# Optimization experiments

Hardware: AMD Instinct MI355X
Metric: run time of the kernel (lower is better)

Reference implementation:

```python
import jax, jax.numpy as jnp
import numpy as np

H = 4  # num_heads (hard-coded in module)
RATION = 5


def setup_inputs() -> dict:
    key = jax.random.key(0)
    ks = jax.random.split(key, 14)
    B, T, S, F = 256, 5, 64, 256
    u = 0.05  # keras 'uniform' initializer scale
    d = {}
    d["x"] = jax.random.normal(ks[0], (B, T, S, F), jnp.float32)
    d["atten_bias"] = jax.random.uniform(ks[1], (B, T, S, S), jnp.float32) * 0.1
    d["W_q"] = jax.random.uniform(ks[2], (F, F), jnp.float32, -u, u)
    d["W_v"] = jax.random.uniform(ks[3], (F, F), jnp.float32, -u, u)
    d["W_o"] = jax.random.uniform(ks[4], (F, F), jnp.float32, -u, u)
    d["u_t"] = jax.random.uniform(ks[5], (T,), jnp.float32, -u, u)
    d["dis"] = jax.random.uniform(ks[6], (T, S, S), jnp.float32, -u, u)
    # keep sigma away from 0 to avoid blowing up the Gaussian prior
    d["sigma"] = jax.random.uniform(ks[7], (T, S, 1), jnp.float32, 0.5, 1.0)
    # SE block: fc1 Dense(T*RATION, relu, he_normal), fc2 Dense(T, sigmoid)
    d["fc1_w"] = jax.random.normal(ks[8], (T, T * RATION), jnp.float32) * np.sqrt(2.0 / T).astype(np.float32)
    d["fc1_b"] = jnp.zeros((T * RATION,), jnp.float32)
    d["fc2_w"] = jax.random.normal(ks[9], (T * RATION, T), jnp.float32) * np.sqrt(2.0 / (T * RATION)).astype(np.float32)
    d["fc2_b"] = jnp.zeros((T,), jnp.float32)
    d["bili_w"] = jax.random.uniform(ks[10], (1,), jnp.float32, -u, u)
    return d


def _se_block(o, fc1_w, fc1_b, fc2_w, fc2_b, bili_w):
    # o: [B,T,S,F] -> transpose to [B,S,F,T]; "channel" axis is T
    xt = jnp.transpose(o, (0, 2, 3, 1))
    avg = jnp.mean(xt, axis=(1, 2))  # [B,T]
    mx = jnp.max(xt, axis=(1, 2))    # [B,T]
    se1 = jax.nn.sigmoid(jax.nn.relu(avg @ fc1_w + fc1_b) @ fc2_w + fc2_b)
    se2 = jax.nn.sigmoid(jax.nn.relu(mx @ fc1_w + fc1_b) @ fc2_w + fc2_b)
    w = bili_w  # shape (1,)
    se = (1.0 - w) * se1 + w * se2   # [B,T]
    out = xt * se[:, None, None, :]
    return jnp.transpose(out, (0, 3, 1, 2))  # back to [B,T,S,F]


def reference(x, atten_bias, W_q, W_v, W_o, u_t, dis, sigma, fc1_w, fc1_b, fc2_w, fc2_b, bili_w):
    B, T, S, F = x.shape
    Fh = F // H
    # q, v: project then reshape (row-major split, exactly as TF reshape)
    q = (x @ W_q).reshape(-1, T, S, Fh)          # [H*B, T, S, Fh]
    v = (x @ W_v).reshape(-1, T, S, Fh)          # [H*B, T, S, Fh]
    # k: contract time with u_t, then [B,F,S] -> [H*B, Fh, S]
    k = jnp.einsum('t,btsf->bsf', u_t, x)        # [B, S, F]
    k = jnp.transpose(k, (0, 2, 1)).reshape(-1, Fh, S)  # [H*B, Fh, S]
    score = jnp.einsum('btsf,bfc->btsc', q, k) / jnp.sqrt(jnp.asarray(Fh, x.dtype))
    score = jax.nn.sigmoid(score)                # [H*B, T, S, S]
    score = score - jnp.tile(atten_bias, (H, 1, 1, 1))
    # learned spatial Gaussian prior, broadcast over batch
    prior = (1.0 / (jnp.sqrt(2.0 * jnp.pi) * sigma)) * jnp.exp(-dis ** 2 / (2.0 * sigma ** 2))
    score = score * prior
    # Dropout(0.3) is identity at inference
    score = jnp.sum(score, axis=-2)              # [H*B, T, S]
    atten = v * score[..., None]                 # [H*B, T, S, Fh]
    o = atten.reshape(-1, T, S, F) @ W_o         # [B, T, S, F]
    o = _se_block(o, fc1_w, fc1_b, fc2_w, fc2_b, bili_w)
    return o + x
```

## Files before the change

kernel.cpp:

```cpp
#include <hip/hip_runtime.h>


typedef unsigned short ushort_t;
typedef __attribute__((ext_vector_type(8))) short bf16x8;
typedef __attribute__((ext_vector_type(4))) float f32x4;

__device__ inline ushort_t f2bf(float f) {
  unsigned u = __float_as_uint(f);
  return (ushort_t)((u + 0x7FFFu + ((u >> 16) & 1u)) >> 16);
}
__device__ inline float bflo(unsigned u) { return __uint_as_float(u << 16); }
__device__ inline float bfhi(unsigned u) { return __uint_as_float(u & 0xFFFF0000u); }

__global__ __launch_bounds__(256) void prior_kernel(const float* __restrict__ dis,
                                                    const float* __restrict__ sigma,
                                                    float* __restrict__ prior) {
  int i = blockIdx.x * 256 + threadIdx.x;
  if (i >= 5 * 64 * 64) return;
  int ts = i >> 6;
  float sg = sigma[ts];
  float d = dis[i];
  prior[i] = 0.3989422804014327f / sg * __expf(-d * d / (2.f * sg * sg));
}

__global__ __launch_bounds__(256) void bias_prior_sum(const float* __restrict__ bias,
                                                      const float* __restrict__ prior,
                                                      float* __restrict__ bps) {
  int blk = blockIdx.x;
  int t = blk % 5, tid = threadIdx.x;
  const float* bp = bias + (size_t)blk * 4096;
  const float* pp = prior + t * 4096;
  int c = tid & 63, sg = tid >> 6;
  float sum = 0.f;
  for (int s = sg * 16; s < sg * 16 + 16; ++s)
    sum += bp[s * 64 + c] * pp[s * 64 + c];
  __shared__ float red[4][64];
  red[sg][c] = sum;
  __syncthreads();
  if (tid < 64)
    bps[(size_t)blk * 64 + tid] = red[0][tid] + red[1][tid] + red[2][tid] + red[3][tid];
}

__global__ __launch_bounds__(256) void k_kernel(const float* __restrict__ x,
                                                const float* __restrict__ u,
                                                ushort_t* __restrict__ kout,
                                                ushort_t* __restrict__ xb) {
  int i = blockIdx.x * 256 + threadIdx.x;
  size_t j = (size_t)i * 4;
  int b = (int)(j >> 14);
  int off = (int)(j & 16383);
  const float* xp = x + (size_t)b * 81920 + off;
  ushort_t* xq = xb + (size_t)b * 81920 + off;
  float u0 = u[0], u1 = u[1], u2 = u[2], u3 = u[3], u4 = u[4];
  float4 a0 = *(const float4*)(xp);
  float4 a1 = *(const float4*)(xp + 16384);
  float4 a2 = *(const float4*)(xp + 32768);
  float4 a3 = *(const float4*)(xp + 49152);
  float4 a4 = *(const float4*)(xp + 65536);
  ushort4 h0 = {f2bf(a0.x), f2bf(a0.y), f2bf(a0.z), f2bf(a0.w)};
  ushort4 h1 = {f2bf(a1.x), f2bf(a1.y), f2bf(a1.z), f2bf(a1.w)};
  ushort4 h2 = {f2bf(a2.x), f2bf(a2.y), f2bf(a2.z), f2bf(a2.w)};
  ushort4 h3 = {f2bf(a3.x), f2bf(a3.y), f2bf(a3.z), f2bf(a3.w)};
  ushort4 h4 = {f2bf(a4.x), f2bf(a4.y), f2bf(a4.z), f2bf(a4.w)};
  *(ushort4*)(xq) = h0;
  *(ushort4*)(xq + 16384) = h1;
  *(ushort4*)(xq + 32768) = h2;
  *(ushort4*)(xq + 49152) = h3;
  *(ushort4*)(xq + 65536) = h4;
  float4 r;
  r.x = u0 * a0.x + u1 * a1.x + u2 * a2.x + u3 * a3.x + u4 * a4.x;
  r.y = u0 * a0.y + u1 * a1.y + u2 * a2.y + u3 * a3.y + u4 * a4.y;
  r.z = u0 * a0.z + u1 * a1.z + u2 * a2.z + u3 * a3.z + u4 * a4.z;
  r.w = u0 * a0.w + u1 * a1.w + u2 * a2.w + u3 * a3.w + u4 * a4.w;
  ushort4 h = {f2bf(r.x), f2bf(r.y), f2bf(r.z), f2bf(r.w)};
  *(ushort4*)(kout + j) = h;
}

__global__ __launch_bounds__(256) void convert_w(const float* __restrict__ Wq,
                                                 const float* __restrict__ Wv,
                                                 const float* __restrict__ Wo,
                                                 ushort_t* __restrict__ Wt) {
  int id = blockIdx.x * 256 + threadIdx.x;
  if (id >= 196608) return;
  int mat = id >> 16, rem = id & 65535;
  int n = rem >> 8, k = rem & 255;
  const float* W = mat == 0 ? Wq : (mat == 1 ? Wv : Wo);
  Wt[id] = f2bf(W[k * 256 + n]);
}

template<int SCALE, int SEEPI>
__global__ __launch_bounds__(512, 4) void gemm_mfma(
    const ushort_t* __restrict__ A, const ushort_t* __restrict__ Wt,
    ushort_t* __restrict__ C, const float* __restrict__ ssum,
    float* __restrict__ ravg, float* __restrict__ rmax) {
  __shared__ __align__(16) ushort_t As_[128 * 64];
  __shared__ __align__(16) ushort_t Bs_[256 * 64];
  __shared__ float redS[8], redM[8];
  const int tid = threadIdx.x;
  const int lane = tid & 63;
  const int w = tid >> 6, wr = w >> 2, wc = w & 3;
  const int row0 = blockIdx.x * 128;
  const int cl = lane & 15, ql = lane >> 4, l7 = lane & 7;

  f32x4 acc[4][4];
#pragma unroll
  for (int i = 0; i < 4; ++i)
#pragma unroll
    for (int j = 0; j < 4; ++j) acc[i][j] = (f32x4){0.f, 0.f, 0.f, 0.f};

  for (int t = 0; t < 4; ++t) {
    const int k0 = t * 64;
    if (t) __syncthreads();
#pragma unroll
    for (int l = 0; l < 2; ++l) {
      int i = l * 512 + tid;
      int r = i >> 3, c = i & 7;
      uint4 v = *(const uint4*)(A + (size_t)(row0 + r) * 256 + k0 + c * 8);
      *(uint4*)&As_[r * 64 + ((c ^ (r & 7)) * 8)] = v;
    }
#pragma unroll
    for (int l = 0; l < 4; ++l) {
      int i = l * 512 + tid;
      int n = i >> 3, c = i & 7;
      uint4 v = *(const uint4*)(Wt + (size_t)n * 256 + k0 + c * 8);
      *(uint4*)&Bs_[n * 64 + ((c ^ (n & 7)) * 8)] = v;
    }
    __syncthreads();
#pragma unroll
    for (int kk = 0; kk < 2; ++kk) {
      const int offk = (((kk << 2) | ql) ^ l7) * 8;
      bf16x8 bfr[4], afr[4];
#pragma unroll
      for (int ni = 0; ni < 4; ++ni)
        bfr[ni] = *(const bf16x8*)&Bs_[(wc * 64 + ni * 16 + cl) * 64 + offk];
#pragma unroll
      for (int mi = 0; mi < 4; ++mi)
        afr[mi] = *(const bf16x8*)&As_[(wr * 64 + mi * 16 + cl) * 64 + offk];
#pragma unroll
      for (int mi = 0; mi < 4; ++mi)
#pragma unroll
        for (int ni = 0; ni < 4; ++ni)
          acc[mi][ni] = __builtin_amdgcn_mfma_f32_16x16x32_bf16(afr[mi], bfr[ni], acc[mi][ni], 0, 0, 0);
    }
  }
  float lsum = 0.f, lmax = -3.4e38f;
#pragma unroll
  for (int mi = 0; mi < 4; ++mi) {
    float sc[4];
    if (SCALE) {
#pragma unroll
      for (int r = 0; r < 4; ++r)
        sc[r] = ssum[(size_t)(row0 + wr * 64 + mi * 16 + ql * 4 + r) * 4 + wc];
    }
#pragma unroll
    for (int ni = 0; ni < 4; ++ni) {
      int col = wc * 64 + ni * 16 + cl;
      f32x4 v = acc[mi][ni];
#pragma unroll
      for (int r = 0; r < 4; ++r) {
        int row = row0 + wr * 64 + mi * 16 + ql * 4 + r;
        float f = v[r];
        if (SCALE) f *= sc[r];
        C[(size_t)row * 256 + col] = f2bf(f);
        if (SEEPI) { lsum += f; lmax = fmaxf(lmax, f); }
      }
    }
  }
  if (SEEPI) {
#pragma unroll
    for (int off = 32; off; off >>= 1) {
      lsum += __shfl_xor(lsum, off);
      lmax = fmaxf(lmax, __shfl_xor(lmax, off));
    }
    if (lane == 0) { redS[w] = lsum; redM[w] = lmax; }
    __syncthreads();
    if (tid < 2) {
      float s = redS[tid * 4] + redS[tid * 4 + 1] + redS[tid * 4 + 2] + redS[tid * 4 + 3];
      float m = fmaxf(fmaxf(redM[tid * 4], redM[tid * 4 + 1]),
                      fmaxf(redM[tid * 4 + 2], redM[tid * 4 + 3]));
      ravg[blockIdx.x * 2 + tid] = s * (1.f / 16384.f);
      rmax[blockIdx.x * 2 + tid] = m;
    }
  }
}

__global__ __launch_bounds__(256) void score_mfma(const ushort_t* __restrict__ q,
                                                  const ushort_t* __restrict__ kbuf,
                                                  const float* __restrict__ prior,
                                                  const float* __restrict__ bps,
                                                  float* __restrict__ ssum) {
  const int n = blockIdx.x;
  const int tid = threadIdx.x;
  const int lane = tid & 63;
  const int w = tid >> 6;
  const int cl = lane & 15, ql = lane >> 4;
  const int nb = n & 255;
  const int c = w * 16 + cl;
  const ushort_t* kb = kbuf + (size_t)(n >> 2) * 16384 + (n & 3) * 64;
  bf16x8 kfr0 = *(const bf16x8*)(kb + c * 256 + ql * 8);
  bf16x8 kfr1 = *(const bf16x8*)(kb + c * 256 + ql * 8 + 32);
  for (int t = 0; t < 5; ++t) {
    const ushort_t* qt = q + (size_t)n * 20480 + t * 4096;
    f32x4 acc[4];
#pragma unroll
    for (int si = 0; si < 4; ++si) {
      bf16x8 a0 = *(const bf16x8*)(qt + (si * 16 + cl) * 64 + ql * 8);
      bf16x8 a1 = *(const bf16x8*)(qt + (si * 16 + cl) * 64 + ql * 8 + 32);
      f32x4 z = (f32x4){0.f, 0.f, 0.f, 0.f};
      z = __builtin_amdgcn_mfma_f32_16x16x32_bf16(a0, kfr0, z, 0, 0, 0);
      z = __builtin_amdgcn_mfma_f32_16x16x32_bf16(a1, kfr1, z, 0, 0, 0);
      acc[si] = z;
    }
    const float* pp = prior + t * 4096;
    float colsum = 0.f;
#pragma unroll
    for (int si = 0; si < 4; ++si) {
#pragma unroll
      for (int r = 0; r < 4; ++r) {
        int s = si * 16 + ql * 4 + r;
        float sg = 1.f / (1.f + __expf(-acc[si][r] * 0.125f));
        colsum += sg * pp[s * 64 + c];
      }
    }
    colsum += __shfl_xor(colsum, 16);
    colsum += __shfl_xor(colsum, 32);
    if (ql == 0)
      ssum[(size_t)n * 320 + t * 64 + c] = colsum - bps[((size_t)nb * 5 + t) * 64 + c];
  }
}

__global__ __launch_bounds__(256) void se_mlp(const float* __restrict__ ravg,
                                              const float* __restrict__ rmax,
                                              const float* __restrict__ fc1w,
                                              const float* __restrict__ fc1b,
                                              const float* __restrict__ fc2w,
                                              const float* __restrict__ fc2b,
                                              const float* __restrict__ bili,
                                              float* __restrict__ se) {
  int b = threadIdx.x;
  float avg[5], mx[5];
  for (int t = 0; t < 5; ++t) { avg[t] = ravg[b * 5 + t]; mx[t] = rmax[b * 5 + t]; }
  float w = bili[0];
  float h[25], s1[5], s2[5];
  for (int j = 0; j < 25; ++j) {
    float a = fc1b[j];
    for (int t = 0; t < 5; ++t) a += avg[t] * fc1w[t * 25 + j];
    h[j] = fmaxf(a, 0.f);
  }
  for (int t = 0; t < 5; ++t) {
    float a = fc2b[t];
    for (int j = 0; j < 25; ++j) a += h[j] * fc2w[j * 5 + t];
    s1[t] = 1.f / (1.f + __expf(-a));
  }
  for (int j = 0; j < 25; ++j) {
    float a = fc1b[j];
    for (int t = 0; t < 5; ++t) a += mx[t] * fc1w[t * 25 + j];
    h[j] = fmaxf(a, 0.f);
  }
  for (int t = 0; t < 5; ++t) {
    float a = fc2b[t];
    for (int j = 0; j < 25; ++j) a += h[j] * fc2w[j * 5 + t];
    s2[t] = 1.f / (1.f + __expf(-a));
  }
  for (int t = 0; t < 5; ++t) se[b * 5 + t] = (1.f - w) * s1[t] + w * s2[t];
}

__global__ __launch_bounds__(256) void final_kernel(const float* __restrict__ x,
                                                    const float* __restrict__ se,
                                                    const ushort_t* __restrict__ ob,
                                                    float* __restrict__ out) {
  int i = blockIdx.x * 256 + threadIdx.x;
  size_t j = (size_t)i * 4;
  int bt = (int)(j >> 14);
  float s = se[bt];
  uint2 u = *(const uint2*)(ob + j);
  float4 xv = *(const float4*)(x + j);
  float4 r = {bflo(u.x) * s + xv.x, bfhi(u.x) * s + xv.y,
              bflo(u.y) * s + xv.z, bfhi(u.y) * s + xv.w};
  *(float4*)(out + j) = r;
}

extern "C" void kernel_launch(void* const* d_in, const int* in_sizes, int n_in,
                              void* d_out, int out_size, void* d_ws, size_t ws_size,
                              hipStream_t stream) {
  const float* x     = (const float*)d_in[0];
  const float* bias  = (const float*)d_in[1];
  const float* Wq    = (const float*)d_in[2];
  const float* Wv    = (const float*)d_in[3];
  const float* Wo    = (const float*)d_in[4];
  const float* u_t   = (const float*)d_in[5];
  const float* dis   = (const float*)d_in[6];
  const float* sigma = (const float*)d_in[7];
  const float* fc1w  = (const float*)d_in[8];
  const float* fc1b  = (const float*)d_in[9];
  const float* fc2w  = (const float*)d_in[10];
  const float* fc2b  = (const float*)d_in[11];
  const float* bili  = (const float*)d_in[12];
  float* out = (float*)d_out;

  char* wsb = (char*)d_ws;
  ushort_t* qvb  = (ushort_t*)wsb;             wsb += 41943040;
  ushort_t* xob  = (ushort_t*)wsb;             wsb += 41943040;
  ushort_t* kb   = (ushort_t*)wsb;             wsb += 8388608;
  ushort_t* Wt   = (ushort_t*)wsb;             wsb += 393216;
  float*    ssum = (float*)wsb;                wsb += 1310720;
  float*    prior= (float*)wsb;                wsb += 81920;
  float*    bps  = (float*)wsb;                wsb += 327680;
  float*    ravg = (float*)wsb;                wsb += 5120;
  float*    rmax = (float*)wsb;                wsb += 5120;
  float*    se   = (float*)wsb;                wsb += 5120;

  convert_w<<<768, 256, 0, stream>>>(Wq, Wv, Wo, Wt);
  prior_kernel<<<80, 256, 0, stream>>>(dis, sigma, prior);
  bias_prior_sum<<<1280, 256, 0, stream>>>(bias, prior, bps);
  k_kernel<<<4096, 256, 0, stream>>>(x, u_t, kb, xob);
  gemm_mfma<0, 0><<<640, 512, 0, stream>>>(xob, Wt, qvb, nullptr, nullptr, nullptr);
  score_mfma<<<1024, 256, 0, stream>>>(qvb, kb, prior, bps, ssum);
  gemm_mfma<1, 0><<<640, 512, 0, stream>>>(xob, Wt + 65536, qvb, ssum, nullptr, nullptr);
  gemm_mfma<0, 1><<<640, 512, 0, stream>>>(qvb, Wt + 131072, xob, nullptr, ravg, rmax);
  se_mlp<<<1, 256, 0, stream>>>(ravg, rmax, fc1w, fc1b, fc2w, fc2b, bili, se);
  final_kernel<<<20480, 256, 0, stream>>>(x, se, xob, out);
}
```

Baseline: 172.3 us.

## Fuse Q projection into score kernel and chain V and O GEMMs in LDS

The Q projection GEMM now runs inside the score kernel, with the per-block Q tile kept in shared memory, so Q is never written to global memory. The V projection (scaled by ssum) and the O projection are chained in one kernel through a swizzled LDS tile, which removes the intermediate V round-trip and one launch. The final residual reads the bf16 copy of x instead of fp32 x, which cuts traffic but adds bf16 rounding error to the residual term. The GEMMs now read operands straight from global memory without LDS staging, and the 64KB LDS tile in vo_gemm may lower occupancy.

```diff
diff --git a/kernel.cpp b/kernel.cpp
--- a/kernel.cpp
+++ b/kernel.cpp
@@ -88,144 +88,183 @@
   Wt[id] = f2bf(W[k * 256 + n]);
 }
 
-template<int SCALE, int SEEPI>
-__global__ __launch_bounds__(512, 4) void gemm_mfma(
-    const ushort_t* __restrict__ A, const ushort_t* __restrict__ Wt,
-    ushort_t* __restrict__ C, const float* __restrict__ ssum,
-    float* __restrict__ ravg, float* __restrict__ rmax) {
-  __shared__ __align__(16) ushort_t As_[128 * 64];
-  __shared__ __align__(16) ushort_t Bs_[256 * 64];
+__global__ __launch_bounds__(256) void qscore(const ushort_t* __restrict__ xb,
+                                              const ushort_t* __restrict__ Wtq,
+                                              const ushort_t* __restrict__ kbuf,
+                                              const float* __restrict__ prior,
+                                              const float* __restrict__ bps,
+                                              float* __restrict__ ssum) {
+  __shared__ __align__(16) ushort_t qlds[5 * 64 * 72];
+  const int n = blockIdx.x;
+  const int tid = threadIdx.x;
+  const int lane = tid & 63, w = tid >> 6;
+  const int cl = lane & 15, ql = lane >> 4;
+  const ushort_t* A = xb + (size_t)n * 20480;
+
+  f32x4 acc[5][4];
+#pragma unroll
+  for (int mi = 0; mi < 5; ++mi)
+#pragma unroll
+    for (int ni = 0; ni < 4; ++ni) acc[mi][ni] = (f32x4){0.f, 0.f, 0.f, 0.f};
+
+#pragma unroll
+  for (int kk = 0; kk < 8; ++kk) {
+    bf16x8 bfr[4];
+#pragma unroll
+    for (int ni = 0; ni < 4; ++ni)
+      bfr[ni] = *(const bf16x8*)(Wtq + (size_t)(w * 64 + ni * 16 + cl) * 256 + kk * 32 + ql * 8);
+#pragma unroll
+    for (int mi = 0; mi < 5; ++mi) {
+      bf16x8 afr = *(const bf16x8*)(A + (size_t)(mi * 16 + cl) * 256 + kk * 32 + ql * 8);
+#pragma unroll
+      for (int ni = 0; ni < 4; ++ni)
+        acc[mi][ni] = __builtin_amdgcn_mfma_f32_16x16x32_bf16(afr, bfr[ni], acc[mi][ni], 0, 0, 0);
+    }
+  }
+#pragma unroll
+  for (int mi = 0; mi < 5; ++mi)
+#pragma unroll
+    for (int ni = 0; ni < 4; ++ni)
+#pragma unroll
+      for (int rr = 0; rr < 4; ++rr)
+        qlds[(mi * 64 + 16 * ql + 4 * rr + w) * 72 + ni * 16 + cl] = f2bf(acc[mi][ni][rr]);
+  __syncthreads();
+
+  const int c = w * 16 + cl;
+  const int nb = n & 255;
+  const ushort_t* kbp = kbuf + (size_t)(n >> 2) * 16384 + (n & 3) * 64;
+  bf16x8 kfr0 = *(const bf16x8*)(kbp + c * 256 + ql * 8);
+  bf16x8 kfr1 = *(const bf16x8*)(kbp + c * 256 + ql * 8 + 32);
+#pragma unroll
+  for (int t = 0; t < 5; ++t) {
+    f32x4 sacc[4];
+#pragma unroll
+    for (int si = 0; si < 4; ++si) {
+      bf16x8 a0 = *(const bf16x8*)&qlds[(t * 64 + si * 16 + cl) * 72 + ql * 8];
+      bf16x8 a1 = *(const bf16x8*)&qlds[(t * 64 + si * 16 + cl) * 72 + ql * 8 + 32];
+      f32x4 z = (f32x4){0.f, 0.f, 0.f, 0.f};
+      z = __builtin_amdgcn_mfma_f32_16x16x32_bf16(a0, kfr0, z, 0, 0, 0);
+      z = __builtin_amdgcn_mfma_f32_16x16x32_bf16(a1, kfr1, z, 0, 0, 0);
+      sacc[si] = z;
+    }
+    const float* pp = prior + t * 4096;
+    float colsum = 0.f;
+#pragma unroll
+    for (int si = 0; si < 4; ++si) {
+#pragma unroll
+      for (int r = 0; r < 4; ++r) {
+        int s = si * 16 + ql * 4 + r;
+        float sg = 1.f / (1.f + __expf(-sacc[si][r] * 0.125f));
+        colsum += sg * pp[s * 64 + c];
+      }
+    }
+    colsum += __shfl_xor(colsum, 16);
+    colsum += __shfl_xor(colsum, 32);
+    if (ql == 0)
+      ssum[(size_t)n * 320 + t * 64 + c] = colsum - bps[((size_t)nb * 5 + t) * 64 + c];
+  }
+}
+
+__global__ __launch_bounds__(512, 2) void vo_gemm(const ushort_t* __restrict__ xb,
+                                                  const ushort_t* __restrict__ Wtv,
+                                                  const ushort_t* __restrict__ Wto,
+                                                  const float* __restrict__ ssum,
+                                                  ushort_t* __restrict__ ob,
+                                                  float* __restrict__ ravg,
+                                                  float* __restrict__ rmax) {
+  __shared__ __align__(16) ushort_t Vs[128 * 256];
   __shared__ float redS[8], redM[8];
   const int tid = threadIdx.x;
   const int lane = tid & 63;
   const int w = tid >> 6, wr = w >> 2, wc = w & 3;
+  const int cl = lane & 15, ql = lane >> 4;
   const int row0 = blockIdx.x * 128;
-  const int cl = lane & 15, ql = lane >> 4, l7 = lane & 7;
 
   f32x4 acc[4][4];
 #pragma unroll
-  for (int i = 0; i < 4; ++i)
-#pragma unroll
-    for (int j = 0; j < 4; ++j) acc[i][j] = (f32x4){0.f, 0.f, 0.f, 0.f};
-
-  for (int t = 0; t < 4; ++t) {
-    const int k0 = t * 64;
-    if (t) __syncthreads();
-#pragma unroll
-    for (int l = 0; l < 2; ++l) {
-      int i = l * 512 + tid;
-      int r = i >> 3, c = i & 7;
-      uint4 v = *(const uint4*)(A + (size_t)(row0 + r) * 256 + k0 + c * 8);
-      *(uint4*)&As_[r * 64 + ((c ^ (r & 7)) * 8)] = v;
-    }
-#pragma unroll
-    for (int l = 0; l < 4; ++l) {
-      int i = l * 512 + tid;
-      int n = i >> 3, c = i & 7;
-      uint4 v = *(const uint4*)(Wt + (size_t)n * 256 + k0 + c * 8);
-      *(uint4*)&Bs_[n * 64 + ((c ^ (n & 7)) * 8)] = v;
-    }
-    __syncthreads();
-#pragma unroll
-    for (int kk = 0; kk < 2; ++kk) {
-      const int offk = (((kk << 2) | ql) ^ l7) * 8;
-      bf16x8 bfr[4], afr[4];
+  for (int mi = 0; mi < 4; ++mi)
+#pragma unroll
+    for (int ni = 0; ni < 4; ++ni) acc[mi][ni] = (f32x4){0.f, 0.f, 0.f, 0.f};
+
+#pragma unroll
+  for (int kk = 0; kk < 8; ++kk) {
+    bf16x8 bfr[4];
+#pragma unroll
+    for (int ni = 0; ni < 4; ++ni)
+      bfr[ni] = *(const bf16x8*)(Wtv + (size_t)(wc * 64 + ni * 16 + cl) * 256 + kk * 32 + ql * 8);
+#pragma unroll
+    for (int mi = 0; mi < 4; ++mi) {
+      bf16x8 afr = *(const bf16x8*)(xb + (size_t)(row0 + wr * 64 + mi * 16 + cl) * 256 + kk * 32 + ql * 8);
 #pragma unroll
       for (int ni = 0; ni < 4; ++ni)
-        bfr[ni] = *(const bf16x8*)&Bs_[(wc * 64 + ni * 16 + cl) * 64 + offk];
-#pragma unroll
-      for (int mi = 0; mi < 4; ++mi)
-        afr[mi] = *(const bf16x8*)&As_[(wr * 64 + mi * 16 + cl) * 64 + offk];
-#pragma unroll
-      for (int mi = 0; mi < 4; ++mi)
-#pragma unroll
-        for (int ni = 0; ni < 4; ++ni)
-          acc[mi][ni] = __builtin_amdgcn_mfma_f32_16x16x32_bf16(afr[mi], bfr[ni], acc[mi][ni], 0, 0, 0);
-    }
-  }
-  float lsum = 0.f, lmax = -3.4e38f;
+        acc[mi][ni] = __builtin_amdgcn_mfma_f32_16x16x32_bf16(afr, bfr[ni], acc[mi][ni], 0, 0, 0);
+    }
+  }
 #pragma unroll
   for (int mi = 0; mi < 4; ++mi) {
     float sc[4];
-    if (SCALE) {
-#pragma unroll
-      for (int r = 0; r < 4; ++r)
-        sc[r] = ssum[(size_t)(row0 + wr * 64 + mi * 16 + ql * 4 + r) * 4 + wc];
-    }
+#pragma unroll
+    for (int r = 0; r < 4; ++r)
+      sc[r] = ssum[(size_t)(row0 + wr * 64 + mi * 16 + ql * 4 + r) * 4 + wc];
 #pragma unroll
     for (int ni = 0; ni < 4; ++ni) {
       int col = wc * 64 + ni * 16 + cl;
-      f32x4 v = acc[mi][ni];
+#pragma unroll
+      for (int r = 0; r < 4; ++r) {
+        int row = wr * 64 + mi * 16 + ql * 4 + r;
+        int chunk = (col >> 3) ^ (row & 31);
+        Vs[row * 256 + chunk * 8 + (col & 7)] = f2bf(acc[mi][ni][r] * sc[r]);
+      }
+    }
+  }
+  __syncthreads();
+#pragma unroll
+  for (int mi = 0; mi < 4; ++mi)
+#pragma unroll
+    for (int ni = 0; ni < 4; ++ni) acc[mi][ni] = (f32x4){0.f, 0.f, 0.f, 0.f};
+#pragma unroll
+  for (int kk = 0; kk < 8; ++kk) {
+    bf16x8 bfr[4];
+#pragma unroll
+    for (int ni = 0; ni < 4; ++ni)
+      bfr[ni] = *(const bf16x8*)(Wto + (size_t)(wc * 64 + ni * 16 + cl) * 256 + kk * 32 + ql * 8);
+#pragma unroll
+    for (int mi = 0; mi < 4; ++mi) {
+      int lrow = wr * 64 + mi * 16 + cl;
+      int chunk = (kk * 4 + ql) ^ (lrow & 31);
+      bf16x8 afr = *(const bf16x8*)&Vs[lrow * 256 + chunk * 8];
+#pragma unroll
+      for (int ni = 0; ni < 4; ++ni)
+        acc[mi][ni] = __builtin_amdgcn_mfma_f32_16x16x32_bf16(afr, bfr[ni], acc[mi][ni], 0, 0, 0);
+    }
+  }
+  float lsum = 0.f, lmax = -3.4e38f;
+#pragma unroll
+  for (int mi = 0; mi < 4; ++mi)
+#pragma unroll
+    for (int ni = 0; ni < 4; ++ni) {
+      int col = wc * 64 + ni * 16 + cl;
 #pragma unroll
       for (int r = 0; r < 4; ++r) {
         int row = row0 + wr * 64 + mi * 16 + ql * 4 + r;
-        float f = v[r];
-        if (SCALE) f *= sc[r];
-        C[(size_t)row * 256 + col] = f2bf(f);
-        if (SEEPI) { lsum += f; lmax = fmaxf(lmax, f); }
+        float f = acc[mi][ni][r];
+        ob[(size_t)row * 256 + col] = f2bf(f);
+        lsum += f; lmax = fmaxf(lmax, f);
       }
     }
-  }
-  if (SEEPI) {
-#pragma unroll
-    for (int off = 32; off; off >>= 1) {
-      lsum += __shfl_xor(lsum, off);
-      lmax = fmaxf(lmax, __shfl_xor(lmax, off));
-    }
-    if (lane == 0) { redS[w] = lsum; redM[w] = lmax; }
-    __syncthreads();
-    if (tid < 2) {
-      float s = redS[tid * 4] + redS[tid * 4 + 1] + redS[tid * 4 + 2] + redS[tid * 4 + 3];
-      float m = fmaxf(fmaxf(redM[tid * 4], redM[tid * 4 + 1]),
-                      fmaxf(redM[tid * 4 + 2], redM[tid * 4 + 3]));
-      ravg[blockIdx.x * 2 + tid] = s * (1.f / 16384.f);
-      rmax[blockIdx.x * 2 + tid] = m;
-    }
-  }
-}
-
-__global__ __launch_bounds__(256) void score_mfma(const ushort_t* __restrict__ q,
-                                                  const ushort_t* __restrict__ kbuf,
-                                                  const float* __restrict__ prior,
-                                                  const float* __restrict__ bps,
-                                                  float* __restrict__ ssum) {
-  const int n = blockIdx.x;
-  const int tid = threadIdx.x;
-  const int lane = tid & 63;
-  const int w = tid >> 6;
-  const int cl = lane & 15, ql = lane >> 4;
-  const int nb = n & 255;
-  const int c = w * 16 + cl;
-  const ushort_t* kb = kbuf + (size_t)(n >> 2) * 16384 + (n & 3) * 64;
-  bf16x8 kfr0 = *(const bf16x8*)(kb + c * 256 + ql * 8);
-  bf16x8 kfr1 = *(const bf16x8*)(kb + c * 256 + ql * 8 + 32);
-  for (int t = 0; t < 5; ++t) {
-    const ushort_t* qt = q + (size_t)n * 20480 + t * 4096;
-    f32x4 acc[4];
-#pragma unroll
-    for (int si = 0; si < 4; ++si) {
-      bf16x8 a0 = *(const bf16x8*)(qt + (si * 16 + cl) * 64 + ql * 8);
-      bf16x8 a1 = *(const bf16x8*)(qt + (si * 16 + cl) * 64 + ql * 8 + 32);
-      f32x4 z = (f32x4){0.f, 0.f, 0.f, 0.f};
-      z = __builtin_amdgcn_mfma_f32_16x16x32_bf16(a0, kfr0, z, 0, 0, 0);
-      z = __builtin_amdgcn_mfma_f32_16x16x32_bf16(a1, kfr1, z, 0, 0, 0);
-      acc[si] = z;
-    }
-    const float* pp = prior + t * 4096;
-    float colsum = 0.f;
-#pragma unroll
-    for (int si = 0; si < 4; ++si) {
-#pragma unroll
-      for (int r = 0; r < 4; ++r) {
-        int s = si * 16 + ql * 4 + r;
-        float sg = 1.f / (1.f + __expf(-acc[si][r] * 0.125f));
-        colsum += sg * pp[s * 64 + c];
-      }
-    }
-    colsum += __shfl_xor(colsum, 16);
-    colsum += __shfl_xor(colsum, 32);
-    if (ql == 0)
-      ssum[(size_t)n * 320 + t * 64 + c] = colsum - bps[((size_t)nb * 5 + t) * 64 + c];
+#pragma unroll
+  for (int off = 32; off; off >>= 1) {
+    lsum += __shfl_xor(lsum, off);
+    lmax = fmaxf(lmax, __shfl_xor(lmax, off));
+  }
+  if (lane == 0) { redS[w] = lsum; redM[w] = lmax; }
+  __syncthreads();
+  if (tid < 2) {
+    float s = redS[tid * 4] + redS[tid * 4 + 1] + redS[tid * 4 + 2] + redS[tid * 4 + 3];
+    float m = fmaxf(fmaxf(redM[tid * 4], redM[tid * 4 + 1]),
+                    fmaxf(redM[tid * 4 + 2], redM[tid * 4 + 3]));
+    ravg[blockIdx.x * 2 + tid] = s * (1.f / 16384.f);
+    rmax[blockIdx.x * 2 + tid] = m;
   }
 }
 
@@ -265,7 +304,7 @@
   for (int t = 0; t < 5; ++t) se[b * 5 + t] = (1.f - w) * s1[t] + w * s2[t];
 }
 
-__global__ __launch_bounds__(256) void final_kernel(const float* __restrict__ x,
+__global__ __launch_bounds__(256) void final_kernel(const ushort_t* __restrict__ xb,
                                                     const float* __restrict__ se,
                                                     const ushort_t* __restrict__ ob,
                                                     float* __restrict__ out) {
@@ -273,10 +312,10 @@
   size_t j = (size_t)i * 4;
   int bt = (int)(j >> 14);
   float s = se[bt];
-  uint2 u = *(const uint2*)(ob + j);
-  float4 xv = *(const float4*)(x + j);
-  float4 r = {bflo(u.x) * s + xv.x, bfhi(u.x) * s + xv.y,
-              bflo(u.y) * s + xv.z, bfhi(u.y) * s + xv.w};
+  uint2 uo = *(const uint2*)(ob + j);
+  uint2 ux = *(const uint2*)(xb + j);
+  float4 r = {bflo(uo.x) * s + bflo(ux.x), bfhi(uo.x) * s + bfhi(ux.x),
+              bflo(uo.y) * s + bflo(ux.y), bfhi(uo.y) * s + bfhi(ux.y)};
   *(float4*)(out + j) = r;
 }
 
@@ -299,8 +338,8 @@
   float* out = (float*)d_out;
 
   char* wsb = (char*)d_ws;
-  ushort_t* qvb  = (ushort_t*)wsb;             wsb += 41943040;
-  ushort_t* xob  = (ushort_t*)wsb;             wsb += 41943040;
+  ushort_t* xbuf = (ushort_t*)wsb;             wsb += 41943040;
+  ushort_t* obuf = (ushort_t*)wsb;             wsb += 41943040;
   ushort_t* kb   = (ushort_t*)wsb;             wsb += 8388608;
   ushort_t* Wt   = (ushort_t*)wsb;             wsb += 393216;
   float*    ssum = (float*)wsb;                wsb += 1310720;
@@ -313,11 +352,9 @@
   convert_w<<<768, 256, 0, stream>>>(Wq, Wv, Wo, Wt);
   prior_kernel<<<80, 256, 0, stream>>>(dis, sigma, prior);
   bias_prior_sum<<<1280, 256, 0, stream>>>(bias, prior, bps);
-  k_kernel<<<4096, 256, 0, stream>>>(x, u_t, kb, xob);
-  gemm_mfma<0, 0><<<640, 512, 0, stream>>>(xob, Wt, qvb, nullptr, nullptr, nullptr);
-  score_mfma<<<1024, 256, 0, stream>>>(qvb, kb, prior, bps, ssum);
-  gemm_mfma<1, 0><<<640, 512, 0, stream>>>(xob, Wt + 65536, qvb, ssum, nullptr, nullptr);
-  gemm_mfma<0, 1><<<640, 512, 0, stream>>>(qvb, Wt + 131072, xob, nullptr, ravg, rmax);
+  k_kernel<<<4096, 256, 0, stream>>>(x, u_t, kb, xbuf);
+  qscore<<<1024, 256, 0, stream>>>(xbuf, Wt, kb, prior, bps, ssum);
+  vo_gemm<<<640, 512, 0, stream>>>(xbuf, Wt + 65536, Wt + 131072, ssum, obuf, ravg, rmax);
   se_mlp<<<1, 256, 0, stream>>>(ravg, rmax, fc1w, fc1b, fc2w, fc2b, bili, se);
-  final_kernel<<<20480, 256, 0, stream>>>(x, se, xob, out);
-}
+  final_kernel<<<20480, 256, 0, stream>>>(xbuf, se, obuf, out);
+}
```

New measurement: 206.7 us. 19.9% more time.
